# Optimization experiments

Hardware: AMD Instinct MI355X
Metric: run time of the kernel (lower is better)

Reference implementation:

```python
import jax, jax.numpy as jnp
import numpy as np

B, H, LQ, LKV, D = 2, 4, 512, 512, 64


def setup_inputs() -> dict:
    key = jax.random.key(0)
    ks = jax.random.split(key, 6)
    queries = jax.random.normal(ks[0], (B, H, LQ, D), dtype=jnp.float32)
    keys = jax.random.normal(ks[1], (B, H, LKV, D), dtype=jnp.float32)
    values = jax.random.normal(ks[2], (B, H, LKV, D), dtype=jnp.float32)
    mask = jax.random.randint(ks[3], (B, LQ, LKV), 0, 2) > 0  # bool [B, Lq, Lkv]
    # linear_concat: weight [D, 2D] (normal std=0.02), bias zeros
    W_concat = jax.random.normal(ks[4], (D, 2 * D), dtype=jnp.float32) * 0.02
    b_concat = jnp.zeros((D,), dtype=jnp.float32)
    # linear_logit: weight [1, D] -> vector [D], bias scalar zero
    w_logit = jax.random.normal(ks[5], (D,), dtype=jnp.float32) * 0.02
    b_logit = jnp.zeros((), dtype=jnp.float32)
    return dict(queries=queries, keys=keys, values=values, mask=mask,
                W_concat=W_concat, b_concat=b_concat,
                w_logit=w_logit, b_logit=b_logit)


def reference(queries, keys, values, mask, W_concat, b_concat, w_logit, b_logit):
    d = queries.shape[-1]
    # cat(q, k) @ W.T == q @ W[:, :d].T + k @ W[:, d:].T  (exact split of the concat-linear)
    qp = jnp.einsum('bhqd,ed->bhqe', queries, W_concat[:, :d])   # [B,H,Lq,D]
    kp = jnp.einsum('bhkd,ed->bhke', keys, W_concat[:, d:])      # [B,H,Lkv,D]
    combined = jnp.tanh(qp[:, :, :, None, :] + kp[:, :, None, :, :] + b_concat)  # [B,H,Lq,Lkv,D]
    logits = jnp.einsum('bhqke,e->bhqk', combined, w_logit) + b_logit            # [B,H,Lq,Lkv]
    # mask handling: invert; rows fully masked get un-masked (avoid all -inf softmax)
    inv = ~mask  # [B,Lq,Lkv]
    inv = jnp.where(jnp.all(inv, axis=-1, keepdims=True), False, inv)
    inv = inv[:, None, :, :]  # broadcast over heads
    logits = jnp.where(inv, -jnp.inf, logits)
    weights = jax.nn.softmax(logits, axis=-1)
    if weights.shape[1] == 1:  # torch .squeeze(dim=1) semantics
        weights = jnp.squeeze(weights, axis=1)
    return weights
```

## Files before the change

### kernel.cpp

```cpp
#include <hip/hip_runtime.h>
#include <hip/hip_bf16.h>


#define NQROWS 4096

__global__ __launch_bounds__(256) void proj_kernel(
    const float* __restrict__ Q, const float* __restrict__ K,
    const float* __restrict__ W, const float* __restrict__ bC,
    float* __restrict__ eq, float* __restrict__ ekt)
{
  const int t  = threadIdx.x;
  const int tr = t >> 6;
  const int e  = t & 63;
  const int rbase = blockIdx.x * 8;
  const bool isK = rbase >= NQROWS;
  const int r0 = isK ? rbase - NQROWS : rbase;
  const float* __restrict__ src = isK ? K : Q;
  const int off = isK ? 64 : 0;

  __shared__ float  srow[8][64];
  __shared__ float4 wsh[64][16];
  __shared__ float  trsp[64][9];

  for (int i = t; i < 8 * 64; i += 256)
    srow[i >> 6][i & 63] = src[(r0 + (i >> 6)) * 64 + (i & 63)];
  for (int i = t; i < 64 * 16; i += 256) {
    const int er = i >> 4, d4 = i & 15;
    wsh[er][d4 ^ (er & 7)] =
        reinterpret_cast<const float4*>(W + er * 128 + off)[d4];
  }
  __syncthreads();

  float acc0 = 0.f, acc1 = 0.f;
  const int rA = tr * 2;
  #pragma unroll
  for (int d4 = 0; d4 < 16; ++d4) {
    const float4 w4 = wsh[e][d4 ^ (e & 7)];
    const float4 s0 = *reinterpret_cast<const float4*>(&srow[rA + 0][d4 * 4]);
    const float4 s1 = *reinterpret_cast<const float4*>(&srow[rA + 1][d4 * 4]);
    acc0 = fmaf(s0.x, w4.x, acc0); acc0 = fmaf(s0.y, w4.y, acc0);
    acc0 = fmaf(s0.z, w4.z, acc0); acc0 = fmaf(s0.w, w4.w, acc0);
    acc1 = fmaf(s1.x, w4.x, acc1); acc1 = fmaf(s1.y, w4.y, acc1);
    acc1 = fmaf(s1.z, w4.z, acc1); acc1 = fmaf(s1.w, w4.w, acc1);
  }

  const float C2 = 2.8853900817779268f;
  if (!isK) {
    const float bias = bC[e];
    eq[(r0 + rA + 0) * 64 + e] = __builtin_amdgcn_exp2f((acc0 + bias) * C2);
    eq[(r0 + rA + 1) * 64 + e] = __builtin_amdgcn_exp2f((acc1 + bias) * C2);
  } else {
    trsp[e][rA + 0] = __builtin_amdgcn_exp2f(acc0 * C2);
    trsp[e][rA + 1] = __builtin_amdgcn_exp2f(acc1 * C2);
    __syncthreads();
    const int bh = r0 >> 9;
    const int k0 = r0 & 511;
    float* __restrict__ dst = ekt + bh * 64 * 512 + k0;
    #pragma unroll
    for (int iter = 0; iter < 2; ++iter) {
      const int i  = t + iter * 256;
      const int e2 = i >> 3, kk = i & 7;
      dst[e2 * 512 + kk] = trsp[e2][kk];
    }
  }
}

__global__ __launch_bounds__(512, 8) void attn_kernel(
    const float* __restrict__ eq, const float* __restrict__ ekt,
    const float* __restrict__ wl, const int* __restrict__ mask,
    float* __restrict__ out)
{
  const int t  = threadIdx.x;
  const int w  = t >> 6;
  const int tk = t & 63;
  const int rw = w >> 1;
  const int h  = w & 1;
  const int bh = blockIdx.x & 7;
  const int qb = blockIdx.x >> 3;
  const int b  = bh >> 2;
  const int q  = qb * 4 + rw;

  __shared__ float qsh[4][64];
  __shared__ float w2s[64];
  __shared__ float s_any[8], s_mmax[8], s_rmax[8], s_sum[8];

  if (t < 64) w2s[t] = -2.0f * wl[t];
  if (h == 0) qsh[rw][tk] = eq[(bh * 512 + q) * 64 + tk];

  const int* __restrict__ mrow = mask + (b * 512 + q) * 512 + h * 256;
  const int4 mv = *reinterpret_cast<const int4*>(mrow + 4 * tk);

  __syncthreads();

  const float4* __restrict__ kq =
      reinterpret_cast<const float4*>(ekt + bh * 64 * 512) + h * 64 + tk;

  float4 acc = {0.f, 0.f, 0.f, 0.f};

#define QUADC(C)                                                              \
  {                                                                           \
    const float t0 = fmaf(q4.x, K0.C, 1.f);                                   \
    const float t1 = fmaf(q4.y, K1.C, 1.f);                                   \
    const float t2 = fmaf(q4.z, K2.C, 1.f);                                   \
    const float t3 = fmaf(q4.w, K3.C, 1.f);                                   \
    const float t01 = t0 * t1, t23 = t2 * t3;                                 \
    const float den = t01 * t23;                                              \
    const float n01 = fmaf(w4.x, t1, w4.y * t0);                              \
    const float n23 = fmaf(w4.z, t3, w4.w * t2);                              \
    const float num = fmaf(n01, t23, n23 * t01);                              \
    acc.C = fmaf(num, __builtin_amdgcn_rcpf(den), acc.C);                     \
  }

  float4 K0 = kq[0 * 128], K1 = kq[1 * 128], K2 = kq[2 * 128], K3 = kq[3 * 128];
  #pragma unroll
  for (int eb = 0; eb < 15; ++eb) {
    const float4 N0 = kq[(eb * 4 + 4) * 128];
    const float4 N1 = kq[(eb * 4 + 5) * 128];
    const float4 N2 = kq[(eb * 4 + 6) * 128];
    const float4 N3 = kq[(eb * 4 + 7) * 128];
    const float4 q4 = *reinterpret_cast<const float4*>(&qsh[rw][eb * 4]);
    const float4 w4 = *reinterpret_cast<const float4*>(&w2s[eb * 4]);
    QUADC(x) QUADC(y) QUADC(z) QUADC(w)
    K0 = N0; K1 = N1; K2 = N2; K3 = N3;
  }
  {
    const float4 q4 = *reinterpret_cast<const float4*>(&qsh[rw][60]);
    const float4 w4 = *reinterpret_cast<const float4*>(&w2s[60]);
    QUADC(x) QUADC(y) QUADC(z) QUADC(w)
  }

  const int lo = mv.x | mv.y | mv.z | mv.w;
  const float hany = __any(lo != 0) ? 1.0f : 0.0f;

  const float NEG = -__builtin_inff();
  float4 am = acc;
  if (mv.x == 0) am.x = NEG;
  if (mv.y == 0) am.y = NEG;
  if (mv.z == 0) am.z = NEG;
  if (mv.w == 0) am.w = NEG;

  float rmax = fmaxf(fmaxf(acc.x, acc.y), fmaxf(acc.z, acc.w));
  float mmax = fmaxf(fmaxf(am.x, am.y), fmaxf(am.z, am.w));
  #pragma unroll
  for (int s = 1; s < 64; s <<= 1) {
    rmax = fmaxf(rmax, __shfl_xor(rmax, s));
    mmax = fmaxf(mmax, __shfl_xor(mmax, s));
  }
  if (tk == 0) { s_any[w] = hany; s_mmax[w] = mmax; s_rmax[w] = rmax; }
  __syncthreads();

  const int wp = w & ~1;
  const bool rowany = (s_any[wp] + s_any[wp + 1]) > 0.0f;
  const float m = rowany ? fmaxf(s_mmax[wp], s_mmax[wp + 1])
                         : fmaxf(s_rmax[wp], s_rmax[wp + 1]);
  const float4 av = rowany ? am : acc;

  const float L2E = 1.4426950408889634f;
  const float c = m * L2E;
  float4 p;
  p.x = __builtin_amdgcn_exp2f(fmaf(av.x, L2E, -c));
  p.y = __builtin_amdgcn_exp2f(fmaf(av.y, L2E, -c));
  p.z = __builtin_amdgcn_exp2f(fmaf(av.z, L2E, -c));
  p.w = __builtin_amdgcn_exp2f(fmaf(av.w, L2E, -c));
  float sum = p.x + p.y + p.z + p.w;
  #pragma unroll
  for (int s = 1; s < 64; s <<= 1) sum += __shfl_xor(sum, s);
  if (tk == 0) s_sum[w] = sum;
  __syncthreads();

  const float inv = 1.0f / (s_sum[wp] + s_sum[wp + 1]);
  float4 o4 = {p.x * inv, p.y * inv, p.z * inv, p.w * inv};
  float* __restrict__ o = out + (bh * 512 + q) * 512 + h * 256;
  *reinterpret_cast<float4*>(o + 4 * tk) = o4;
}

extern "C" void kernel_launch(void* const* d_in, const int* in_sizes, int n_in,
                              void* d_out, int out_size, void* d_ws, size_t ws_size,
                              hipStream_t stream) {
  const float* Q  = (const float*)d_in[0];
  const float* K  = (const float*)d_in[1];
  const int*   M  = (const int*)d_in[3];
  const float* W  = (const float*)d_in[4];
  const float* bC = (const float*)d_in[5];
  const float* wl = (const float*)d_in[6];
  float* out = (float*)d_out;
  float* eqbuf  = (float*)d_ws;
  float* ektbuf = eqbuf + NQROWS * 64;

  proj_kernel<<<1024, 256, 0, stream>>>(Q, K, W, bC, eqbuf, ektbuf);
  attn_kernel<<<1024, 512, 0, stream>>>(eqbuf, ektbuf, wl, M, out);
}
```

Measured before the change: 29.72 us.

## Compute two query rows per thread and drop max-subtraction in attention softmax

Each thread now handles two query rows over four key columns, so every loaded key float4 is reused across two rows. The block shrinks to 256 threads, and the key software-prefetch is replaced by a plain unroll-4 loop. The softmax skips the row-max pass: it exponentiates the logits directly and builds masked and unmasked sums in a single reduction, removing one block barrier and one shuffle round. This is safe only because the logits are bounded (absolute value at most twice the sum of absolute logit weights), and it raises register pressure because two accumulators are live per thread.

Result: faster. 25.21 us, median of 2 (-15.2%).

```diff
diff --git a/kernel.cpp b/kernel.cpp
--- a/kernel.cpp
+++ b/kernel.cpp
@@ -65,113 +65,122 @@
   }
 }
 
-__global__ __launch_bounds__(512, 8) void attn_kernel(
+__global__ __launch_bounds__(256) void attn_kernel(
     const float* __restrict__ eq, const float* __restrict__ ekt,
     const float* __restrict__ wl, const int* __restrict__ mask,
     float* __restrict__ out)
 {
   const int t  = threadIdx.x;
-  const int w  = t >> 6;
-  const int tk = t & 63;
-  const int rw = w >> 1;
-  const int h  = w & 1;
+  const int g  = t >> 7;
+  const int c  = t & 127;
+  const int wv = t >> 6;
+  const int ln = t & 63;
   const int bh = blockIdx.x & 7;
-  const int qb = blockIdx.x >> 3;
+  const int qg = blockIdx.x >> 3;
   const int b  = bh >> 2;
-  const int q  = qb * 4 + rw;
+  const int q0 = qg * 4;
+  const int r0 = q0 + g * 2;
 
   __shared__ float qsh[4][64];
   __shared__ float w2s[64];
-  __shared__ float s_any[8], s_mmax[8], s_rmax[8], s_sum[8];
+  __shared__ float s_sm[4][2], s_sr[4][2];
+  __shared__ int   s_any[4][2];
 
   if (t < 64) w2s[t] = -2.0f * wl[t];
-  if (h == 0) qsh[rw][tk] = eq[(bh * 512 + q) * 64 + tk];
-
-  const int* __restrict__ mrow = mask + (b * 512 + q) * 512 + h * 256;
-  const int4 mv = *reinterpret_cast<const int4*>(mrow + 4 * tk);
-
+  qsh[t >> 6][t & 63] = eq[(bh * 512 + q0 + (t >> 6)) * 64 + (t & 63)];
   __syncthreads();
 
   const float4* __restrict__ kq =
-      reinterpret_cast<const float4*>(ekt + bh * 64 * 512) + h * 64 + tk;
-
-  float4 acc = {0.f, 0.f, 0.f, 0.f};
-
-#define QUADC(C)                                                              \
+      reinterpret_cast<const float4*>(ekt + bh * 64 * 512) + c;
+
+  float4 a0 = {0.f, 0.f, 0.f, 0.f};
+  float4 a1 = {0.f, 0.f, 0.f, 0.f};
+
+#define QUADC(AC, QV, C)                                                      \
   {                                                                           \
-    const float t0 = fmaf(q4.x, K0.C, 1.f);                                   \
-    const float t1 = fmaf(q4.y, K1.C, 1.f);                                   \
-    const float t2 = fmaf(q4.z, K2.C, 1.f);                                   \
-    const float t3 = fmaf(q4.w, K3.C, 1.f);                                   \
+    const float t0 = fmaf(QV.x, K0.C, 1.f);                                   \
+    const float t1 = fmaf(QV.y, K1.C, 1.f);                                   \
+    const float t2 = fmaf(QV.z, K2.C, 1.f);                                   \
+    const float t3 = fmaf(QV.w, K3.C, 1.f);                                   \
     const float t01 = t0 * t1, t23 = t2 * t3;                                 \
     const float den = t01 * t23;                                              \
     const float n01 = fmaf(w4.x, t1, w4.y * t0);                              \
     const float n23 = fmaf(w4.z, t3, w4.w * t2);                              \
     const float num = fmaf(n01, t23, n23 * t01);                              \
-    acc.C = fmaf(num, __builtin_amdgcn_rcpf(den), acc.C);                     \
-  }
-
-  float4 K0 = kq[0 * 128], K1 = kq[1 * 128], K2 = kq[2 * 128], K3 = kq[3 * 128];
-  #pragma unroll
-  for (int eb = 0; eb < 15; ++eb) {
-    const float4 N0 = kq[(eb * 4 + 4) * 128];
-    const float4 N1 = kq[(eb * 4 + 5) * 128];
-    const float4 N2 = kq[(eb * 4 + 6) * 128];
-    const float4 N3 = kq[(eb * 4 + 7) * 128];
-    const float4 q4 = *reinterpret_cast<const float4*>(&qsh[rw][eb * 4]);
+    AC.C = fmaf(num, __builtin_amdgcn_rcpf(den), AC.C);                       \
+  }
+#define QROW(AC, QV) QUADC(AC, QV, x) QUADC(AC, QV, y) \
+                     QUADC(AC, QV, z) QUADC(AC, QV, w)
+
+  #pragma unroll 4
+  for (int eb = 0; eb < 16; ++eb) {
+    const float4 K0 = kq[(eb * 4 + 0) * 128];
+    const float4 K1 = kq[(eb * 4 + 1) * 128];
+    const float4 K2 = kq[(eb * 4 + 2) * 128];
+    const float4 K3 = kq[(eb * 4 + 3) * 128];
+    const float4 qa = *reinterpret_cast<const float4*>(&qsh[g * 2 + 0][eb * 4]);
+    const float4 qb = *reinterpret_cast<const float4*>(&qsh[g * 2 + 1][eb * 4]);
     const float4 w4 = *reinterpret_cast<const float4*>(&w2s[eb * 4]);
-    QUADC(x) QUADC(y) QUADC(z) QUADC(w)
-    K0 = N0; K1 = N1; K2 = N2; K3 = N3;
-  }
-  {
-    const float4 q4 = *reinterpret_cast<const float4*>(&qsh[rw][60]);
-    const float4 w4 = *reinterpret_cast<const float4*>(&w2s[60]);
-    QUADC(x) QUADC(y) QUADC(z) QUADC(w)
-  }
-
-  const int lo = mv.x | mv.y | mv.z | mv.w;
-  const float hany = __any(lo != 0) ? 1.0f : 0.0f;
-
-  const float NEG = -__builtin_inff();
-  float4 am = acc;
-  if (mv.x == 0) am.x = NEG;
-  if (mv.y == 0) am.y = NEG;
-  if (mv.z == 0) am.z = NEG;
-  if (mv.w == 0) am.w = NEG;
-
-  float rmax = fmaxf(fmaxf(acc.x, acc.y), fmaxf(acc.z, acc.w));
-  float mmax = fmaxf(fmaxf(am.x, am.y), fmaxf(am.z, am.w));
+    QROW(a0, qa) QROW(a1, qb)
+  }
+
+  const int* __restrict__ mb = mask + (b * 512 + r0) * 512 + 4 * c;
+  const int4 mv0 = *reinterpret_cast<const int4*>(mb);
+  const int4 mv1 = *reinterpret_cast<const int4*>(mb + 512);
+
+  const float L2E = 1.4426950408889634f;
+  float4 p0, p1;
+  p0.x = __builtin_amdgcn_exp2f(a0.x * L2E);
+  p0.y = __builtin_amdgcn_exp2f(a0.y * L2E);
+  p0.z = __builtin_amdgcn_exp2f(a0.z * L2E);
+  p0.w = __builtin_amdgcn_exp2f(a0.w * L2E);
+  p1.x = __builtin_amdgcn_exp2f(a1.x * L2E);
+  p1.y = __builtin_amdgcn_exp2f(a1.y * L2E);
+  p1.z = __builtin_amdgcn_exp2f(a1.z * L2E);
+  p1.w = __builtin_amdgcn_exp2f(a1.w * L2E);
+
+  float sm0 = ((mv0.x ? p0.x : 0.f) + (mv0.y ? p0.y : 0.f)) +
+              ((mv0.z ? p0.z : 0.f) + (mv0.w ? p0.w : 0.f));
+  float sm1 = ((mv1.x ? p1.x : 0.f) + (mv1.y ? p1.y : 0.f)) +
+              ((mv1.z ? p1.z : 0.f) + (mv1.w ? p1.w : 0.f));
+  float sr0 = (p0.x + p0.y) + (p0.z + p0.w);
+  float sr1 = (p1.x + p1.y) + (p1.z + p1.w);
+  const int any0 = __any((mv0.x | mv0.y | mv0.z | mv0.w) != 0) ? 1 : 0;
+  const int any1 = __any((mv1.x | mv1.y | mv1.z | mv1.w) != 0) ? 1 : 0;
+
   #pragma unroll
   for (int s = 1; s < 64; s <<= 1) {
-    rmax = fmaxf(rmax, __shfl_xor(rmax, s));
-    mmax = fmaxf(mmax, __shfl_xor(mmax, s));
-  }
-  if (tk == 0) { s_any[w] = hany; s_mmax[w] = mmax; s_rmax[w] = rmax; }
+    sm0 += __shfl_xor(sm0, s); sm1 += __shfl_xor(sm1, s);
+    sr0 += __shfl_xor(sr0, s); sr1 += __shfl_xor(sr1, s);
+  }
+  if (ln == 0) {
+    s_sm[wv][0] = sm0; s_sm[wv][1] = sm1;
+    s_sr[wv][0] = sr0; s_sr[wv][1] = sr1;
+    s_any[wv][0] = any0; s_any[wv][1] = any1;
+  }
   __syncthreads();
 
-  const int wp = w & ~1;
-  const bool rowany = (s_any[wp] + s_any[wp + 1]) > 0.0f;
-  const float m = rowany ? fmaxf(s_mmax[wp], s_mmax[wp + 1])
-                         : fmaxf(s_rmax[wp], s_rmax[wp + 1]);
-  const float4 av = rowany ? am : acc;
-
-  const float L2E = 1.4426950408889634f;
-  const float c = m * L2E;
-  float4 p;
-  p.x = __builtin_amdgcn_exp2f(fmaf(av.x, L2E, -c));
-  p.y = __builtin_amdgcn_exp2f(fmaf(av.y, L2E, -c));
-  p.z = __builtin_amdgcn_exp2f(fmaf(av.z, L2E, -c));
-  p.w = __builtin_amdgcn_exp2f(fmaf(av.w, L2E, -c));
-  float sum = p.x + p.y + p.z + p.w;
-  #pragma unroll
-  for (int s = 1; s < 64; s <<= 1) sum += __shfl_xor(sum, s);
-  if (tk == 0) s_sum[w] = sum;
-  __syncthreads();
-
-  const float inv = 1.0f / (s_sum[wp] + s_sum[wp + 1]);
-  float4 o4 = {p.x * inv, p.y * inv, p.z * inv, p.w * inv};
-  float* __restrict__ o = out + (bh * 512 + q) * 512 + h * 256;
-  *reinterpret_cast<float4*>(o + 4 * tk) = o4;
+  const int wA = g * 2, wB = g * 2 + 1;
+  const bool ra0 = (s_any[wA][0] | s_any[wB][0]) != 0;
+  const bool ra1 = (s_any[wA][1] | s_any[wB][1]) != 0;
+  const float inv0 =
+      1.0f / (ra0 ? (s_sm[wA][0] + s_sm[wB][0]) : (s_sr[wA][0] + s_sr[wB][0]));
+  const float inv1 =
+      1.0f / (ra1 ? (s_sm[wA][1] + s_sm[wB][1]) : (s_sr[wA][1] + s_sr[wB][1]));
+
+  float4 o0, o1;
+  o0.x = ((!ra0 || mv0.x) ? p0.x : 0.f) * inv0;
+  o0.y = ((!ra0 || mv0.y) ? p0.y : 0.f) * inv0;
+  o0.z = ((!ra0 || mv0.z) ? p0.z : 0.f) * inv0;
+  o0.w = ((!ra0 || mv0.w) ? p0.w : 0.f) * inv0;
+  o1.x = ((!ra1 || mv1.x) ? p1.x : 0.f) * inv1;
+  o1.y = ((!ra1 || mv1.y) ? p1.y : 0.f) * inv1;
+  o1.z = ((!ra1 || mv1.z) ? p1.z : 0.f) * inv1;
+  o1.w = ((!ra1 || mv1.w) ? p1.w : 0.f) * inv1;
+
+  float* __restrict__ o = out + (bh * 512 + r0) * 512 + 4 * c;
+  *reinterpret_cast<float4*>(o) = o0;
+  *reinterpret_cast<float4*>(o + 512) = o1;
 }
 
 extern "C" void kernel_launch(void* const* d_in, const int* in_sizes, int n_in,
@@ -188,5 +197,5 @@
   float* ektbuf = eqbuf + NQROWS * 64;
 
   proj_kernel<<<1024, 256, 0, stream>>>(Q, K, W, bC, eqbuf, ektbuf);
-  attn_kernel<<<1024, 512, 0, stream>>>(eqbuf, ektbuf, wl, M, out);
+  attn_kernel<<<1024, 256, 0, stream>>>(eqbuf, ektbuf, wl, M, out);
 }
```
